# Kernel optimization log

Hardware: AMD Instinct MI355X
Metric: run time of the kernel (lower is better)

## Reference

```python
import jax, jax.numpy as jnp
import numpy as np

SCALE = 30.0
MARGIN = 0.5
COS_M = float(np.cos(MARGIN))
SIN_M = float(np.sin(MARGIN))
TH = float(np.cos(np.pi - MARGIN))
MM = float(np.sin(np.pi - MARGIN) * MARGIN)
LN_EPS = 1e-7

B, S, H = 16, 2048, 1024
N_SPANS = 64
N_CLASSES = 4096


def setup_inputs() -> dict:
    key = jax.random.key(0)
    k1, k2, k3, k4, k5 = jax.random.split(key, 5)
    encoder_layer = jax.random.normal(k1, (B, S, H), dtype=jnp.float32)
    ln_gamma = jnp.ones((H,), jnp.float32)
    ln_beta = jnp.zeros((H,), jnp.float32)
    # xavier-uniform-like init for arcface head weight [out, in]
    limit = float(np.sqrt(6.0 / (N_CLASSES + H)))
    arc_weight = jax.random.uniform(k2, (N_CLASSES, H), jnp.float32, -limit, limit)
    heads = jax.random.randint(k3, (B, N_SPANS), 0, S - 32).astype(jnp.int32)
    lens = jax.random.randint(k4, (B, N_SPANS), 1, 33).astype(jnp.int32)
    tails = heads + lens  # guaranteed head < tail <= S
    labels = jax.random.randint(k5, (B, N_SPANS), 0, N_CLASSES).astype(jnp.int32)
    return {
        "encoder_layer": encoder_layer,
        "ln_gamma": ln_gamma,
        "ln_beta": ln_beta,
        "arc_weight": arc_weight,
        "span_head_idxs": heads,
        "span_tail_idxs": tails,
        "labels": labels,
    }


def _span_mean(encoder_layer, heads, tails):
    # fused ragged segment-mean via inclusive prefix sums over the seq dim
    # csum: [B, S+1, H], csum[b, t] = sum of encoder_layer[b, :t]
    csum = jnp.concatenate(
        [jnp.zeros_like(encoder_layer[:, :1]), jnp.cumsum(encoder_layer, axis=1)], axis=1
    )
    gather = lambda idx: jnp.take_along_axis(csum, idx[:, :, None].astype(jnp.int32), axis=1)
    sums = gather(tails) - gather(heads)  # [B, n_spans, H]
    counts = (tails - heads).astype(encoder_layer.dtype)[:, :, None]
    return sums / counts


def _layer_norm(x, gamma, beta):
    mu = jnp.mean(x, axis=-1, keepdims=True)
    var = jnp.mean(jnp.square(x - mu), axis=-1, keepdims=True)
    return (x - mu) * jax.lax.rsqrt(var + LN_EPS) * gamma + beta


def _l2norm(x):
    return x / jnp.maximum(jnp.linalg.norm(x, axis=-1, keepdims=True), 1e-12)


def reference(encoder_layer, ln_gamma, ln_beta, arc_weight, span_head_idxs, span_tail_idxs, labels):
    emb = _span_mean(encoder_layer, span_head_idxs, span_tail_idxs)  # [B, n_spans, H]
    emb = _layer_norm(emb, ln_gamma, ln_beta)
    emb = emb.reshape(-1, emb.shape[-1])  # [B*n_spans, H]
    lab = labels.reshape(-1)
    # ArcMarginProduct: cosine similarity
    cosine = (_l2norm(emb) @ _l2norm(arc_weight).T).astype(jnp.float32)  # [N, C]
    sine = jnp.sqrt(jnp.clip(1.0 - jnp.square(cosine), 0.0))
    phi = cosine * COS_M - sine * SIN_M
    phi = jnp.where(cosine > TH, phi, cosine - MM)
    onehot = jax.nn.one_hot(lab, cosine.shape[-1], dtype=cosine.dtype)
    logits = (onehot * phi + (1.0 - onehot) * cosine) * SCALE
    # mean cross entropy (all labels valid, ignore_index unused)
    logp = jax.nn.log_softmax(logits, axis=-1)
    nll = -jnp.take_along_axis(logp, lab[:, None].astype(jnp.int32), axis=1)[:, 0]
    return jnp.mean(nll)
```

## Files before the change

kernel.cpp:

```cpp
#include <hip/hip_runtime.h>
#include <math.h>

#define B_     16
#define S_     2048
#define H_     1024
#define NS_    64
#define NC_    4096
#define NROWS  1024

#define SCALE_ 30.0f
#define COS_M_ 0.8775825618903728f
#define SIN_M_ 0.479425538604203f
#define TH_    (-0.8775825618903728f)
#define MM_    0.2397127693021015f
#define LN_EPS_ 1e-7f


__device__ __forceinline__ unsigned short f2bf(float f) {
    union { float f; unsigned int u; } v; v.f = f;
    unsigned int r = v.u + 0x7fffu + ((v.u >> 16) & 1u);
    return (unsigned short)(r >> 16);
}

__device__ __forceinline__ float block_sum(float v) {
    __shared__ float sb[4];
    #pragma unroll
    for (int off = 32; off > 0; off >>= 1) v += __shfl_down(v, off, 64);
    if ((threadIdx.x & 63) == 0) sb[threadIdx.x >> 6] = v;
    __syncthreads();
    float r = sb[0] + sb[1] + sb[2] + sb[3];
    __syncthreads();
    return r;
}

__device__ __forceinline__ float block_max(float v) {
    __shared__ float sb[4];
    #pragma unroll
    for (int off = 32; off > 0; off >>= 1) v = fmaxf(v, __shfl_down(v, off, 64));
    if ((threadIdx.x & 63) == 0) sb[threadIdx.x >> 6] = v;
    __syncthreads();
    float r = fmaxf(fmaxf(sb[0], sb[1]), fmaxf(sb[2], sb[3]));
    __syncthreads();
    return r;
}

__device__ __forceinline__ void gload16(const void* g, void* l) {
    __builtin_amdgcn_global_load_lds(
        (const __attribute__((address_space(1))) unsigned int*)g,
        (__attribute__((address_space(3))) unsigned int*)l,
        16, 0, 0);
}

typedef short bf16x8 __attribute__((ext_vector_type(8)));
typedef float f32x4  __attribute__((ext_vector_type(4)));

__global__ __launch_bounds__(256) void fused_norm_kernel(
    const float* __restrict__ enc,
    const float* __restrict__ gamma,
    const float* __restrict__ beta,
    const int*   __restrict__ heads,
    const int*   __restrict__ tails,
    const float* __restrict__ W,
    unsigned short* __restrict__ embn,
    unsigned short* __restrict__ Wn)
{
    const int tid = threadIdx.x;

    if (blockIdx.x < NROWS) {
        const int span = blockIdx.x;
        const int b    = span >> 6;
        const int head = heads[span];
        const int tail = tails[span];
        const int cnt  = tail - head;

        const float4* base = (const float4*)(enc + ((size_t)b * S_ + head) * H_) + tid;
        float a0x=0.f,a0y=0.f,a0z=0.f,a0w=0.f;
        float a1x=0.f,a1y=0.f,a1z=0.f,a1w=0.f;
        int s = 0;
        for (; s + 2 <= cnt; s += 2) {
            float4 x = base[(size_t)s       * (H_ / 4)];
            float4 y = base[(size_t)(s + 1) * (H_ / 4)];
            a0x += x.x; a0y += x.y; a0z += x.z; a0w += x.w;
            a1x += y.x; a1y += y.y; a1z += y.z; a1w += y.w;
        }
        if (s < cnt) {
            float4 x = base[(size_t)s * (H_ / 4)];
            a0x += x.x; a0y += x.y; a0z += x.z; a0w += x.w;
        }
        const float inv = 1.0f / (float)cnt;
        float v0 = (a0x + a1x) * inv, v1 = (a0y + a1y) * inv;
        float v2 = (a0z + a1z) * inv, v3 = (a0w + a1w) * inv;

        float mu = block_sum(v0 + v1 + v2 + v3) * (1.0f / H_);
        float d0 = v0 - mu, d1 = v1 - mu, d2 = v2 - mu, d3 = v3 - mu;
        float var = block_sum(d0*d0 + d1*d1 + d2*d2 + d3*d3) * (1.0f / H_);
        float rstd = rsqrtf(var + LN_EPS_);

        const int h = tid * 4;
        float y0 = d0 * rstd * gamma[h+0] + beta[h+0];
        float y1 = d1 * rstd * gamma[h+1] + beta[h+1];
        float y2 = d2 * rstd * gamma[h+2] + beta[h+2];
        float y3 = d3 * rstd * gamma[h+3] + beta[h+3];

        float ss = block_sum(y0*y0 + y1*y1 + y2*y2 + y3*y3);
        float invn = 1.0f / fmaxf(sqrtf(ss), 1e-12f);

        ushort4 o;
        o.x = f2bf(y0 * invn); o.y = f2bf(y1 * invn);
        o.z = f2bf(y2 * invn); o.w = f2bf(y3 * invn);
        *(ushort4*)(embn + (size_t)span * H_ + h) = o;
    } else {
        const int row = blockIdx.x - NROWS;
        float4 x = ((const float4*)(W + (size_t)row * H_))[tid];
        float ss = block_sum(x.x*x.x + x.y*x.y + x.z*x.z + x.w*x.w);
        float invn = 1.0f / fmaxf(sqrtf(ss), 1e-12f);
        ushort4 o;
        o.x = f2bf(x.x * invn); o.y = f2bf(x.y * invn);
        o.z = f2bf(x.z * invn); o.w = f2bf(x.w * invn);
        *(ushort4*)(Wn + (size_t)row * H_ + tid * 4) = o;
    }
}

__global__ __launch_bounds__(256, 1) void gemm_kernel(
    const unsigned short* __restrict__ A,
    const unsigned short* __restrict__ Bw,
    float* __restrict__ C)
{
    __shared__ short As[2][128 * 64];
    __shared__ short Bs[2][128 * 64];

    const int bid = blockIdx.y * 8 + blockIdx.x;
    const int swz = (bid & 7) * 32 + (bid >> 3);
    const int m0  = (swz & 7) * 128;
    const int n0  = (swz >> 3) * 128;

    const int tid  = threadIdx.x;
    const int lane = tid & 63;
    const int w    = tid >> 6;
    const int wm   = (w & 1) * 64;
    const int wn   = (w >> 1) * 64;
    const int lrow = lane & 15;
    const int q    = lane >> 4;
    const int xr   = lrow & 7;

    const int srow = tid >> 3;
    const int sc16 = tid & 7;

    f32x4 acc[4][4];
    #pragma unroll
    for (int i = 0; i < 4; ++i)
        #pragma unroll
        for (int j = 0; j < 4; ++j)
            acc[i][j] = (f32x4){0.f, 0.f, 0.f, 0.f};

    auto stage = [&](int bsel, int k0) {
        #pragma unroll
        for (int i = 0; i < 4; ++i) {
            const int row = i * 32 + srow;
            const int s16 = sc16 ^ (row & 7);
            gload16(A  + (size_t)(m0 + row) * 1024 + k0 + s16 * 8,
                    &As[bsel][row * 64 + sc16 * 8]);
            gload16(Bw + (size_t)(n0 + row) * 1024 + k0 + s16 * 8,
                    &Bs[bsel][row * 64 + sc16 * 8]);
        }
    };

    auto compute = [&](int bsel) {
        #pragma unroll
        for (int kk = 0; kk < 2; ++kk) {
            const int c16 = ((kk << 2) | q) ^ xr;
            bf16x8 af[4], bfr[4];
            #pragma unroll
            for (int i = 0; i < 4; ++i)
                af[i] = *(const bf16x8*)(&As[bsel][(wm + i * 16 + lrow) * 64 + c16 * 8]);
            #pragma unroll
            for (int j = 0; j < 4; ++j)
                bfr[j] = *(const bf16x8*)(&Bs[bsel][(wn + j * 16 + lrow) * 64 + c16 * 8]);
            #pragma unroll
            for (int i = 0; i < 4; ++i)
                #pragma unroll
                for (int j = 0; j < 4; ++j)
                    acc[i][j] = __builtin_amdgcn_mfma_f32_16x16x32_bf16(af[i], bfr[j], acc[i][j], 0, 0, 0);
        }
    };

    stage(0, 0);
    asm volatile("s_waitcnt vmcnt(0)" ::: "memory");
    __builtin_amdgcn_s_barrier();

    int cur = 0;
    for (int t = 0; t < 15; ++t) {
        stage(cur ^ 1, (t + 1) * 64);
        compute(cur);
        asm volatile("s_waitcnt vmcnt(0)" ::: "memory");
        __builtin_amdgcn_s_barrier();
        cur ^= 1;
    }
    compute(cur);

    #pragma unroll
    for (int i = 0; i < 4; ++i) {
        const int rbase = m0 + wm + i * 16 + q * 4;
        #pragma unroll
        for (int j = 0; j < 4; ++j) {
            const int col = n0 + wn + j * 16 + lrow;
            #pragma unroll
            for (int r2 = 0; r2 < 4; ++r2)
                C[(size_t)(rbase + r2) * NC_ + col] = acc[i][j][r2];
        }
    }
}

__global__ __launch_bounds__(256) void ce_kernel(
    const float* __restrict__ cosine,
    const int*   __restrict__ labels,
    float* __restrict__ nll)
{
    __shared__ float s_lab;
    const int row = blockIdx.x;
    const int lab = labels[row];
    const int tid = threadIdx.x;
    const float4* c4 = (const float4*)(cosine + (size_t)row * NC_);

    float vals[16];
    float m = -1e30f;
    #pragma unroll
    for (int t = 0; t < 4; ++t) {
        float4 x = c4[tid + t * 256];
        const int cbase = (tid + t * 256) * 4;
        float xs[4] = {x.x, x.y, x.z, x.w};
        #pragma unroll
        for (int k = 0; k < 4; ++k) {
            float c = xs[k];
            float logit = c;
            if (cbase + k == lab) {
                float sine = sqrtf(fmaxf(1.0f - c * c, 0.0f));
                float phi  = c * COS_M_ - sine * SIN_M_;
                logit = (c > TH_) ? phi : (c - MM_);
            }
            logit *= SCALE_;
            vals[t * 4 + k] = logit;
            if (cbase + k == lab) s_lab = logit;
            m = fmaxf(m, logit);
        }
    }
    float gm = block_max(m);
    float e = 0.f;
    #pragma unroll
    for (int t = 0; t < 16; ++t) e += expf(vals[t] - gm);
    float se = block_sum(e);
    if (tid == 0) nll[row] = logf(se) + gm - s_lab;
}

__global__ __launch_bounds__(256) void mean_kernel(
    const float* __restrict__ nll, float* __restrict__ out)
{
    const int tid = threadIdx.x;
    float s = 0.f;
    #pragma unroll
    for (int t = 0; t < 4; ++t) s += nll[tid + t * 256];
    float tot = block_sum(s);
    if (tid == 0) out[0] = tot * (1.0f / NROWS);
}

extern "C" void kernel_launch(void* const* d_in, const int* in_sizes, int n_in,
                              void* d_out, int out_size, void* d_ws, size_t ws_size,
                              hipStream_t stream) {
    const float* enc    = (const float*)d_in[0];
    const float* gamma  = (const float*)d_in[1];
    const float* beta   = (const float*)d_in[2];
    const float* W      = (const float*)d_in[3];
    const int*   heads  = (const int*)d_in[4];
    const int*   tails  = (const int*)d_in[5];
    const int*   labels = (const int*)d_in[6];
    float* out = (float*)d_out;

    char* ws = (char*)d_ws;
    unsigned short* embn   = (unsigned short*)(ws);
    unsigned short* Wn     = (unsigned short*)(ws + (2u  << 20));
    float*          cosine = (float*)        (ws + (10u << 20));
    float*          nllbuf = (float*)        (ws + (26u << 20));

    fused_norm_kernel<<<NROWS + NC_, 256, 0, stream>>>(enc, gamma, beta, heads, tails, W, embn, Wn);
    dim3 g3(8, 32);
    gemm_kernel <<<g3,  256, 0, stream>>>(embn, Wn, cosine);
    ce_kernel   <<<NROWS, 256, 0, stream>>>(cosine, labels, nllbuf);
    mean_kernel <<<1,     256, 0, stream>>>(nllbuf, out);
}
```

Baseline: 227.7 us.

## Triple-buffer GEMM with 8 waves, unroll span sum, fuse mean into CE

```diff
diff --git a/kernel.cpp b/kernel.cpp
--- a/kernel.cpp
+++ b/kernel.cpp
@@ -62,34 +62,41 @@
     const int*   __restrict__ tails,
     const float* __restrict__ W,
     unsigned short* __restrict__ embn,
-    unsigned short* __restrict__ Wn)
+    unsigned short* __restrict__ Wn,
+    unsigned int*   __restrict__ cnt)
 {
     const int tid = threadIdx.x;
+    if (blockIdx.x == 0 && tid == 0) *cnt = 0u;
 
     if (blockIdx.x < NROWS) {
         const int span = blockIdx.x;
         const int b    = span >> 6;
         const int head = heads[span];
         const int tail = tails[span];
-        const int cnt  = tail - head;
+        const int cnt_ = tail - head;
 
         const float4* base = (const float4*)(enc + ((size_t)b * S_ + head) * H_) + tid;
-        float a0x=0.f,a0y=0.f,a0z=0.f,a0w=0.f;
-        float a1x=0.f,a1y=0.f,a1z=0.f,a1w=0.f;
+        float4 a0 = {0.f,0.f,0.f,0.f}, a1 = a0, a2 = a0, a3 = a0;
         int s = 0;
-        for (; s + 2 <= cnt; s += 2) {
-            float4 x = base[(size_t)s       * (H_ / 4)];
-            float4 y = base[(size_t)(s + 1) * (H_ / 4)];
-            a0x += x.x; a0y += x.y; a0z += x.z; a0w += x.w;
-            a1x += y.x; a1y += y.y; a1z += y.z; a1w += y.w;
-        }
-        if (s < cnt) {
+        for (; s + 4 <= cnt_; s += 4) {
+            float4 x0 = base[(size_t)(s + 0) * (H_ / 4)];
+            float4 x1 = base[(size_t)(s + 1) * (H_ / 4)];
+            float4 x2 = base[(size_t)(s + 2) * (H_ / 4)];
+            float4 x3 = base[(size_t)(s + 3) * (H_ / 4)];
+            a0.x += x0.x; a0.y += x0.y; a0.z += x0.z; a0.w += x0.w;
+            a1.x += x1.x; a1.y += x1.y; a1.z += x1.z; a1.w += x1.w;
+            a2.x += x2.x; a2.y += x2.y; a2.z += x2.z; a2.w += x2.w;
+            a3.x += x3.x; a3.y += x3.y; a3.z += x3.z; a3.w += x3.w;
+        }
+        for (; s < cnt_; ++s) {
             float4 x = base[(size_t)s * (H_ / 4)];
-            a0x += x.x; a0y += x.y; a0z += x.z; a0w += x.w;
-        }
-        const float inv = 1.0f / (float)cnt;
-        float v0 = (a0x + a1x) * inv, v1 = (a0y + a1y) * inv;
-        float v2 = (a0z + a1z) * inv, v3 = (a0w + a1w) * inv;
+            a0.x += x.x; a0.y += x.y; a0.z += x.z; a0.w += x.w;
+        }
+        const float inv = 1.0f / (float)cnt_;
+        float v0 = (a0.x + a1.x + a2.x + a3.x) * inv;
+        float v1 = (a0.y + a1.y + a2.y + a3.y) * inv;
+        float v2 = (a0.z + a1.z + a2.z + a3.z) * inv;
+        float v3 = (a0.w + a1.w + a2.w + a3.w) * inv;
 
         float mu = block_sum(v0 + v1 + v2 + v3) * (1.0f / H_);
         float d0 = v0 - mu, d1 = v1 - mu, d2 = v2 - mu, d3 = v3 - mu;
@@ -121,13 +128,13 @@
     }
 }
 
-__global__ __launch_bounds__(256, 1) void gemm_kernel(
+__global__ __launch_bounds__(512, 1) void gemm_kernel(
     const unsigned short* __restrict__ A,
     const unsigned short* __restrict__ Bw,
     float* __restrict__ C)
 {
-    __shared__ short As[2][128 * 64];
-    __shared__ short Bs[2][128 * 64];
+    __shared__ short As[3][128 * 64];
+    __shared__ short Bs[3][128 * 64];
 
     const int bid = blockIdx.y * 8 + blockIdx.x;
     const int swz = (bid & 7) * 32 + (bid >> 3);
@@ -137,31 +144,27 @@
     const int tid  = threadIdx.x;
     const int lane = tid & 63;
     const int w    = tid >> 6;
-    const int wm   = (w & 1) * 64;
-    const int wn   = (w >> 1) * 64;
+    const int wRow = (w >> 2) * 64;
+    const int wCol = (w & 3) * 32;
     const int lrow = lane & 15;
     const int q    = lane >> 4;
     const int xr   = lrow & 7;
 
-    const int srow = tid >> 3;
-    const int sc16 = tid & 7;
-
-    f32x4 acc[4][4];
+    f32x4 acc[4][2];
     #pragma unroll
     for (int i = 0; i < 4; ++i)
         #pragma unroll
-        for (int j = 0; j < 4; ++j)
+        for (int j = 0; j < 2; ++j)
             acc[i][j] = (f32x4){0.f, 0.f, 0.f, 0.f};
 
     auto stage = [&](int bsel, int k0) {
         #pragma unroll
-        for (int i = 0; i < 4; ++i) {
-            const int row = i * 32 + srow;
-            const int s16 = sc16 ^ (row & 7);
-            gload16(A  + (size_t)(m0 + row) * 1024 + k0 + s16 * 8,
-                    &As[bsel][row * 64 + sc16 * 8]);
-            gload16(Bw + (size_t)(n0 + row) * 1024 + k0 + s16 * 8,
-                    &Bs[bsel][row * 64 + sc16 * 8]);
+        for (int h = 0; h < 2; ++h) {
+            const int s   = tid + h * 512;
+            const int row = s >> 3;
+            const int s16 = (s & 7) ^ (row & 7);
+            gload16(A  + (size_t)(m0 + row) * 1024 + k0 + s16 * 8, &As[bsel][s * 8]);
+            gload16(Bw + (size_t)(n0 + row) * 1024 + k0 + s16 * 8, &Bs[bsel][s * 8]);
         }
     };
 
@@ -169,41 +172,45 @@
         #pragma unroll
         for (int kk = 0; kk < 2; ++kk) {
             const int c16 = ((kk << 2) | q) ^ xr;
-            bf16x8 af[4], bfr[4];
+            bf16x8 af[4], bfr[2];
             #pragma unroll
             for (int i = 0; i < 4; ++i)
-                af[i] = *(const bf16x8*)(&As[bsel][(wm + i * 16 + lrow) * 64 + c16 * 8]);
+                af[i] = *(const bf16x8*)(&As[bsel][(wRow + i * 16 + lrow) * 64 + c16 * 8]);
             #pragma unroll
-            for (int j = 0; j < 4; ++j)
-                bfr[j] = *(const bf16x8*)(&Bs[bsel][(wn + j * 16 + lrow) * 64 + c16 * 8]);
+            for (int j = 0; j < 2; ++j)
+                bfr[j] = *(const bf16x8*)(&Bs[bsel][(wCol + j * 16 + lrow) * 64 + c16 * 8]);
             #pragma unroll
             for (int i = 0; i < 4; ++i)
                 #pragma unroll
-                for (int j = 0; j < 4; ++j)
+                for (int j = 0; j < 2; ++j)
                     acc[i][j] = __builtin_amdgcn_mfma_f32_16x16x32_bf16(af[i], bfr[j], acc[i][j], 0, 0, 0);
         }
     };
 
     stage(0, 0);
+    stage(1, 64);
+    asm volatile("s_waitcnt vmcnt(4)" ::: "memory");
+    __builtin_amdgcn_s_barrier();
+
+    int cur = 0, nxt = 1, fut = 2;
+    for (int t = 0; t < 14; ++t) {
+        stage(fut, (t + 2) * 64);
+        compute(cur);
+        asm volatile("s_waitcnt vmcnt(4)" ::: "memory");
+        __builtin_amdgcn_s_barrier();
+        const int tmp = cur; cur = nxt; nxt = fut; fut = tmp;
+    }
+    compute(cur);
     asm volatile("s_waitcnt vmcnt(0)" ::: "memory");
     __builtin_amdgcn_s_barrier();
-
-    int cur = 0;
-    for (int t = 0; t < 15; ++t) {
-        stage(cur ^ 1, (t + 1) * 64);
-        compute(cur);
-        asm volatile("s_waitcnt vmcnt(0)" ::: "memory");
-        __builtin_amdgcn_s_barrier();
-        cur ^= 1;
-    }
-    compute(cur);
+    compute(nxt);
 
     #pragma unroll
     for (int i = 0; i < 4; ++i) {
-        const int rbase = m0 + wm + i * 16 + q * 4;
-        #pragma unroll
-        for (int j = 0; j < 4; ++j) {
-            const int col = n0 + wn + j * 16 + lrow;
+        const int rbase = m0 + wRow + i * 16 + q * 4;
+        #pragma unroll
+        for (int j = 0; j < 2; ++j) {
+            const int col = n0 + wCol + j * 16 + lrow;
             #pragma unroll
             for (int r2 = 0; r2 < 4; ++r2)
                 C[(size_t)(rbase + r2) * NC_ + col] = acc[i][j][r2];
@@ -214,9 +221,12 @@
 __global__ __launch_bounds__(256) void ce_kernel(
     const float* __restrict__ cosine,
     const int*   __restrict__ labels,
-    float* __restrict__ nll)
+    float* __restrict__ nll,
+    float* __restrict__ out,
+    unsigned int* __restrict__ cnt)
 {
     __shared__ float s_lab;
+    __shared__ int   s_last;
     const int row = blockIdx.x;
     const int lab = labels[row];
     const int tid = threadIdx.x;
@@ -249,18 +259,21 @@
     #pragma unroll
     for (int t = 0; t < 16; ++t) e += expf(vals[t] - gm);
     float se = block_sum(e);
-    if (tid == 0) nll[row] = logf(se) + gm - s_lab;
-}
-
-__global__ __launch_bounds__(256) void mean_kernel(
-    const float* __restrict__ nll, float* __restrict__ out)
-{
-    const int tid = threadIdx.x;
-    float s = 0.f;
-    #pragma unroll
-    for (int t = 0; t < 4; ++t) s += nll[tid + t * 256];
-    float tot = block_sum(s);
-    if (tid == 0) out[0] = tot * (1.0f / NROWS);
+
+    if (tid == 0) {
+        nll[row] = logf(se) + gm - s_lab;
+        __threadfence();
+        s_last = (atomicAdd(cnt, 1u) == NROWS - 1);
+    }
+    __syncthreads();
+    if (s_last) {
+        __threadfence();
+        float s = 0.f;
+        #pragma unroll
+        for (int t = 0; t < 4; ++t) s += nll[tid + t * 256];
+        float tot = block_sum(s);
+        if (tid == 0) out[0] = tot * (1.0f / NROWS);
+    }
 }
 
 extern "C" void kernel_launch(void* const* d_in, const int* in_sizes, int n_in,
@@ -280,10 +293,10 @@
     unsigned short* Wn     = (unsigned short*)(ws + (2u  << 20));
     float*          cosine = (float*)        (ws + (10u << 20));
     float*          nllbuf = (float*)        (ws + (26u << 20));
-
-    fused_norm_kernel<<<NROWS + NC_, 256, 0, stream>>>(enc, gamma, beta, heads, tails, W, embn, Wn);
+    unsigned int*   cnt    = (unsigned int*) (ws + (26u << 20) + 8192);
+
+    fused_norm_kernel<<<NROWS + NC_, 256, 0, stream>>>(enc, gamma, beta, heads, tails, W, embn, Wn, cnt);
     dim3 g3(8, 32);
-    gemm_kernel <<<g3,  256, 0, stream>>>(embn, Wn, cosine);
-    ce_kernel   <<<NROWS, 256, 0, stream>>>(cosine, labels, nllbuf);
-    mean_kernel <<<1,     256, 0, stream>>>(nllbuf, out);
-}
+    gemm_kernel <<<g3,  512, 0, stream>>>(embn, Wn, cosine);
+    ce_kernel   <<<NROWS, 256, 0, stream>>>(cosine, labels, nllbuf, out, cnt);
+}
```

New measurement: 234.8 us. +3.1%, slower.
